# Optimization experiments

Measured on AMD Instinct MI355X. Metric: run time of the kernel, lower is better.

## Reference

```python
import jax, jax.numpy as jnp
import numpy as np


def setup_inputs() -> dict:
    key = jax.random.key(0)
    kq, kk, kv, km, kb = jax.random.split(key, 5)
    B, H, S, D = 4, 16, 2048, 64
    Q = jax.random.normal(kq, (B, H, S, D), dtype=jnp.float32)
    K = jax.random.normal(kk, (B, H, S, D), dtype=jnp.float32)
    V = jax.random.normal(kv, (B, H, S, D), dtype=jnp.float32)
    # key-padding style mask, broadcasts over query dim; 0 -> masked
    mask = jax.random.randint(km, (B, 1, 1, S), 0, 2, dtype=jnp.int32)
    attn_bias = jax.random.normal(kb, (1, H, S, S), dtype=jnp.float32)
    return {"Q": Q, "K": K, "V": V, "mask": mask, "attn_bias": attn_bias}


def reference(Q, K, V, mask, attn_bias):
    d_k = Q.shape[-1]
    scale = 1.0 / jnp.sqrt(jnp.asarray(d_k, Q.dtype))
    # [B,H,Sq,Sk] scores
    scores = jnp.einsum("bhqd,bhkd->bhqk", Q, K) * scale
    scores = scores + attn_bias
    scores = jnp.where(mask == 0, jnp.asarray(-1e9, scores.dtype), scores)
    attn = jax.nn.softmax(scores, axis=-1)
    # dropout is identity in eval/reference mode
    output = jnp.einsum("bhqk,bhkd->bhqd", attn, V)
    return output, attn
```

## Files before the change

### kernel.cpp

```cpp
#include <hip/hip_runtime.h>

#define NB 4
#define NH 16
#define NS 2048
#define ND 64
#define PST 2052

typedef __attribute__((ext_vector_type(8))) short short8;
typedef __attribute__((ext_vector_type(4))) short short4v;
typedef __attribute__((ext_vector_type(4))) float floatx4;
typedef __attribute__((ext_vector_type(2))) float floatx2;

__device__ __forceinline__ unsigned short f2bf(float f) {
  unsigned u = __builtin_bit_cast(unsigned, f);
  u = (u + 0x7FFFu + ((u >> 16) & 1u)) >> 16;
  return (unsigned short)u;
}
__device__ __forceinline__ float bf2f(unsigned short s) {
  unsigned u = ((unsigned)s) << 16;
  return __builtin_bit_cast(float, u);
}

__global__ __launch_bounds__(256) void prep_k_kernel(const float* __restrict__ K,
                                                     unsigned short* __restrict__ kb) {
  size_t i = ((size_t)blockIdx.x * 256 + threadIdx.x) * 4;
  floatx4 v = *(const floatx4*)(K + i);
  unsigned long long o = 0;
  o |= (unsigned long long)f2bf(v[0]);
  o |= (unsigned long long)f2bf(v[1]) << 16;
  o |= (unsigned long long)f2bf(v[2]) << 32;
  o |= (unsigned long long)f2bf(v[3]) << 48;
  *(unsigned long long*)(kb + i) = o;
}

__global__ __launch_bounds__(256) void prep_vt_kernel(const float* __restrict__ V,
                                                      unsigned short* __restrict__ vt) {
  __shared__ float tile[64][65];
  int kc = blockIdx.x & 31;
  int bh = blockIdx.x >> 5;
  int k0 = kc * 64;
  const float* src = V + ((size_t)bh * NS + k0) * ND;
  int t = threadIdx.x;
  int r0 = t >> 4;
  int c = (t & 15) * 4;
  for (int rr = 0; rr < 4; ++rr) {
    int r = rr * 16 + r0;
    floatx4 v = *(const floatx4*)(src + (size_t)r * ND + c);
    tile[r][c + 0] = v[0]; tile[r][c + 1] = v[1];
    tile[r][c + 2] = v[2]; tile[r][c + 3] = v[3];
  }
  __syncthreads();
  unsigned short* dst = vt + (size_t)bh * ND * NS + k0;
  for (int i = 0; i < 16; ++i) {
    int lin = i * 256 + t;
    int d = lin >> 6, k = lin & 63;
    dst[(size_t)d * NS + k] = f2bf(tile[k][d]);
  }
}

__global__ __launch_bounds__(1024, 8) void attn_kernel(
    const float* __restrict__ Q,
    const unsigned short* __restrict__ Kb,
    const unsigned short* __restrict__ VT,
    const int* __restrict__ mask,
    const float* __restrict__ bias,
    float* __restrict__ out,
    float* __restrict__ attn) {
  extern __shared__ char smem[];
  unsigned short* P = (unsigned short*)smem;
  float* sums = (float*)(smem + 16 * PST * 2);

  const int bid = blockIdx.x;
  const int b = bid & 3;
  const int qt = (bid >> 2) & 127;
  const int h = bid >> 9;
  const int q0 = qt * 16;

  const int tid = threadIdx.x;
  const int wave = tid >> 6;
  const int lane = tid & 63;
  const int lg = lane >> 4;
  const int lc = lane & 15;
  const int lg4 = lg * 4;
  const int lg8 = lg * 8;

  const size_t bh = (size_t)(b * NH + h);

  short8 aq[2];
  {
    const float* qrow = Q + (bh * NS + (size_t)(q0 + lc)) * ND + lg8;
#pragma unroll
    for (int t = 0; t < 2; ++t) {
      floatx4 f0 = *(const floatx4*)(qrow + t * 32);
      floatx4 f1 = *(const floatx4*)(qrow + t * 32 + 4);
      short8 a;
      a[0] = (short)f2bf(f0[0]); a[1] = (short)f2bf(f0[1]);
      a[2] = (short)f2bf(f0[2]); a[3] = (short)f2bf(f0[3]);
      a[4] = (short)f2bf(f1[0]); a[5] = (short)f2bf(f1[1]);
      a[6] = (short)f2bf(f1[2]); a[7] = (short)f2bf(f1[3]);
      aq[t] = a;
    }
  }

  const unsigned short* kp = Kb + bh * NS * ND + (size_t)lc * ND + lg8;
  const float* bprow = bias + ((size_t)h * NS + (size_t)(q0 + lg4)) * NS + lc;
  const int* mp = mask + b * NS + lc;

  float psum[4] = {0.f, 0.f, 0.f, 0.f};
  const int kb0 = wave * 128;

  short8 kfa[2], kfb[2];
  float bvv[2][4];
  int mvv[2];
  {
    const int k0 = kb0;
    kfa[0] = *(const short8*)(kp + (size_t)k0 * ND);
    kfb[0] = *(const short8*)(kp + (size_t)k0 * ND + 32);
    mvv[0] = mp[k0];
#pragma unroll
    for (int r = 0; r < 4; ++r) bvv[0][r] = bprow[(size_t)r * NS + k0];
  }
#pragma unroll
  for (int it = 0; it < 8; ++it) {
    const int cur = it & 1, nxt = cur ^ 1;
    if (it < 7) {
      const int k1 = kb0 + (it + 1) * 16;
      kfa[nxt] = *(const short8*)(kp + (size_t)k1 * ND);
      kfb[nxt] = *(const short8*)(kp + (size_t)k1 * ND + 32);
      mvv[nxt] = mp[k1];
#pragma unroll
      for (int r = 0; r < 4; ++r) bvv[nxt][r] = bprow[(size_t)r * NS + k1];
    }
    const int k0 = kb0 + it * 16;
    floatx4 c = {0.f, 0.f, 0.f, 0.f};
    c = __builtin_amdgcn_mfma_f32_16x16x32_bf16(aq[0], kfa[cur], c, 0, 0, 0);
    c = __builtin_amdgcn_mfma_f32_16x16x32_bf16(aq[1], kfb[cur], c, 0, 0, 0);
#pragma unroll
    for (int r = 0; r < 4; ++r) {
      float s = c[r] * 0.125f + bvv[cur][r];
      float p = mvv[cur] ? __expf(s) : 0.f;
      psum[r] += p;
      P[(lg4 + r) * PST + k0 + lc] = f2bf(p);
    }
  }

#pragma unroll
  for (int r = 0; r < 4; ++r) {
    float v = psum[r];
    v += __shfl_xor(v, 1);
    v += __shfl_xor(v, 2);
    v += __shfl_xor(v, 4);
    v += __shfl_xor(v, 8);
    if (lc == 0) sums[wave * 16 + lg4 + r] = v;
  }
  __syncthreads();

  {
    const int row = wave;
    float tot = 0.f;
#pragma unroll
    for (int w = 0; w < 16; ++w) tot += sums[w * 16 + row];
    const float inv = 1.f / tot;
    float* arow = attn + (bh * NS + (size_t)(q0 + row)) * NS;
    const unsigned short* prow = P + row * PST;
#pragma unroll
    for (int it = 0; it < 8; ++it) {
      const int col = it * 256 + lane * 4;
      short4v pv = *(const short4v*)(prow + col);
      floatx4 f;
      f[0] = bf2f((unsigned short)pv[0]) * inv;
      f[1] = bf2f((unsigned short)pv[1]) * inv;
      f[2] = bf2f((unsigned short)pv[2]) * inv;
      f[3] = bf2f((unsigned short)pv[3]) * inv;
      __builtin_nontemporal_store(f, (floatx4*)(arow + col));
    }
  }

  floatx4 o[4];
#pragma unroll
  for (int dt = 0; dt < 4; ++dt) o[dt] = (floatx4){0.f, 0.f, 0.f, 0.f};

  const unsigned short* vp = VT + bh * (size_t)ND * NS + (size_t)lc * NS + lg8;
#pragma unroll
  for (int it = 0; it < 4; ++it) {
    const int k0 = kb0 + it * 32;
    const unsigned short* pr = P + lc * PST + k0 + lg8;
    short4v lo = *(const short4v*)pr;
    short4v hi = *(const short4v*)(pr + 4);
    short8 pa = __builtin_shufflevector(lo, hi, 0, 1, 2, 3, 4, 5, 6, 7);
#pragma unroll
    for (int dt = 0; dt < 4; ++dt) {
      short8 bb = *(const short8*)(vp + (size_t)(dt * 16) * NS + k0);
      o[dt] = __builtin_amdgcn_mfma_f32_16x16x32_bf16(pa, bb, o[dt], 0, 0, 0);
    }
  }
  __syncthreads();

  float* Ored = (float*)smem;
#pragma unroll
  for (int dt = 0; dt < 4; ++dt)
#pragma unroll
    for (int r = 0; r < 4; ++r)
      Ored[((size_t)wave * 16 + lg4 + r) * 64 + dt * 16 + lc] = o[dt][r];
  __syncthreads();

  {
    const int q = tid >> 6;
    const int col = tid & 63;
    float acc = 0.f;
#pragma unroll
    for (int w = 0; w < 16; ++w) acc += Ored[((size_t)w * 16 + q) * 64 + col];
    float tot = 0.f;
#pragma unroll
    for (int w = 0; w < 16; ++w) tot += sums[w * 16 + q];
    const float inv = 1.f / tot;
    __builtin_nontemporal_store(acc * inv, out + (bh * NS + (size_t)(q0 + q)) * ND + col);
  }
}

extern "C" void kernel_launch(void* const* d_in, const int* in_sizes, int n_in,
                              void* d_out, int out_size, void* d_ws, size_t ws_size,
                              hipStream_t stream) {
  const float* Q = (const float*)d_in[0];
  const float* K = (const float*)d_in[1];
  const float* V = (const float*)d_in[2];
  const int* mask = (const int*)d_in[3];
  const float* bias = (const float*)d_in[4];

  float* out = (float*)d_out;
  float* attn = out + (size_t)NB * NH * NS * ND;

  unsigned short* kb = (unsigned short*)d_ws;
  unsigned short* vt = kb + (size_t)NB * NH * NS * ND;

  const int lds_bytes = 16 * PST * 2 + 16 * 16 * 4;
  (void)hipFuncSetAttribute((const void*)attn_kernel,
                            hipFuncAttributeMaxDynamicSharedMemorySize, lds_bytes);

  prep_k_kernel<<<(NB * NH * NS * ND) / (256 * 4), 256, 0, stream>>>(K, kb);
  prep_vt_kernel<<<NB * NH * (NS / 64), 256, 0, stream>>>(V, vt);
  attn_kernel<<<NB * NH * (NS / 16), 1024, lds_bytes, stream>>>(Q, kb, vt, mask, bias, out, attn);
}
```

Baseline: 738.8 us.

## Halve waves per block, deepen K prefetch, interleave attn writes with PV MFMAs

The attention kernel now launches 512 threads (8 waves) per block, so each wave covers 256 keys instead of 128. The score loop uses a 4-slot register ring that prefetches K, bias and mask three steps ahead, where it used to double-buffer. The normalized attention-row stores are interleaved with the P·V MFMAs and double-buffered V^T loads, so the attn write stream overlaps compute. The final reduction reads 8 partials and writes two floats per thread. The trade-off is higher register pressure per wave and fewer waves per block to hide latency.

```diff
diff --git a/kernel.cpp b/kernel.cpp
--- a/kernel.cpp
+++ b/kernel.cpp
@@ -58,7 +58,7 @@
   }
 }
 
-__global__ __launch_bounds__(1024, 8) void attn_kernel(
+__global__ __launch_bounds__(512, 4) void attn_kernel(
     const float* __restrict__ Q,
     const unsigned short* __restrict__ Kb,
     const unsigned short* __restrict__ VT,
@@ -105,40 +105,47 @@
   const unsigned short* kp = Kb + bh * NS * ND + (size_t)lc * ND + lg8;
   const float* bprow = bias + ((size_t)h * NS + (size_t)(q0 + lg4)) * NS + lc;
   const int* mp = mask + b * NS + lc;
+  const int kb0 = wave * 256;
 
   float psum[4] = {0.f, 0.f, 0.f, 0.f};
-  const int kb0 = wave * 128;
-
-  short8 kfa[2], kfb[2];
-  float bvv[2][4];
-  int mvv[2];
-  {
-    const int k0 = kb0;
-    kfa[0] = *(const short8*)(kp + (size_t)k0 * ND);
-    kfb[0] = *(const short8*)(kp + (size_t)k0 * ND + 32);
-    mvv[0] = mp[k0];
-#pragma unroll
-    for (int r = 0; r < 4; ++r) bvv[0][r] = bprow[(size_t)r * NS + k0];
-  }
-#pragma unroll
-  for (int it = 0; it < 8; ++it) {
-    const int cur = it & 1, nxt = cur ^ 1;
-    if (it < 7) {
-      const int k1 = kb0 + (it + 1) * 16;
-      kfa[nxt] = *(const short8*)(kp + (size_t)k1 * ND);
-      kfb[nxt] = *(const short8*)(kp + (size_t)k1 * ND + 32);
-      mvv[nxt] = mp[k1];
-#pragma unroll
-      for (int r = 0; r < 4; ++r) bvv[nxt][r] = bprow[(size_t)r * NS + k1];
+
+  short8 rka[4], rkb[4];
+  floatx4 rbv[4];
+  int rmv[4];
+#pragma unroll
+  for (int i = 0; i < 3; ++i) {
+    const int k0 = kb0 + i * 16;
+    rka[i] = *(const short8*)(kp + (size_t)k0 * ND);
+    rkb[i] = *(const short8*)(kp + (size_t)k0 * ND + 32);
+    rmv[i] = mp[k0];
+    floatx4 bv;
+#pragma unroll
+    for (int r = 0; r < 4; ++r) bv[r] = bprow[(size_t)r * NS + k0];
+    rbv[i] = bv;
+  }
+#pragma unroll
+  for (int it = 0; it < 16; ++it) {
+    const int s = it & 3;
+    if (it < 13) {
+      const int ps = (it + 3) & 3;
+      const int k1 = kb0 + (it + 3) * 16;
+      rka[ps] = *(const short8*)(kp + (size_t)k1 * ND);
+      rkb[ps] = *(const short8*)(kp + (size_t)k1 * ND + 32);
+      rmv[ps] = mp[k1];
+      floatx4 bv;
+#pragma unroll
+      for (int r = 0; r < 4; ++r) bv[r] = bprow[(size_t)r * NS + k1];
+      rbv[ps] = bv;
     }
     const int k0 = kb0 + it * 16;
     floatx4 c = {0.f, 0.f, 0.f, 0.f};
-    c = __builtin_amdgcn_mfma_f32_16x16x32_bf16(aq[0], kfa[cur], c, 0, 0, 0);
-    c = __builtin_amdgcn_mfma_f32_16x16x32_bf16(aq[1], kfb[cur], c, 0, 0, 0);
+    c = __builtin_amdgcn_mfma_f32_16x16x32_bf16(aq[0], rka[s], c, 0, 0, 0);
+    c = __builtin_amdgcn_mfma_f32_16x16x32_bf16(aq[1], rkb[s], c, 0, 0, 0);
+    const int mv = rmv[s];
 #pragma unroll
     for (int r = 0; r < 4; ++r) {
-      float s = c[r] * 0.125f + bvv[cur][r];
-      float p = mvv[cur] ? __expf(s) : 0.f;
+      float sc = c[r] * 0.125f + rbv[s][r];
+      float p = mv ? __expf(sc) : 0.f;
       psum[r] += p;
       P[(lg4 + r) * PST + k0 + lc] = f2bf(p);
     }
@@ -155,25 +162,34 @@
   }
   __syncthreads();
 
+  const int wrow0 = wave * 2;
+  float inv0, inv1;
   {
-    const int row = wave;
-    float tot = 0.f;
-#pragma unroll
-    for (int w = 0; w < 16; ++w) tot += sums[w * 16 + row];
-    const float inv = 1.f / tot;
-    float* arow = attn + (bh * NS + (size_t)(q0 + row)) * NS;
-    const unsigned short* prow = P + row * PST;
-#pragma unroll
-    for (int it = 0; it < 8; ++it) {
-      const int col = it * 256 + lane * 4;
-      short4v pv = *(const short4v*)(prow + col);
-      floatx4 f;
-      f[0] = bf2f((unsigned short)pv[0]) * inv;
-      f[1] = bf2f((unsigned short)pv[1]) * inv;
-      f[2] = bf2f((unsigned short)pv[2]) * inv;
-      f[3] = bf2f((unsigned short)pv[3]) * inv;
-      __builtin_nontemporal_store(f, (floatx4*)(arow + col));
-    }
+    float t0 = 0.f, t1 = 0.f;
+#pragma unroll
+    for (int w = 0; w < 8; ++w) {
+      t0 += sums[w * 16 + wrow0];
+      t1 += sums[w * 16 + wrow0 + 1];
+    }
+    inv0 = 1.f / t0;
+    inv1 = 1.f / t1;
+  }
+
+  const size_t abase = (bh * NS + (size_t)q0) * NS;
+
+#define WRITECHUNK(c)                                                        \
+  {                                                                          \
+    const int row_ = wrow0 + ((c) >> 3);                                     \
+    const float inv_ = (((c) >> 3) == 0) ? inv0 : inv1;                      \
+    const int col_ = ((c) & 7) * 256 + lane * 4;                             \
+    short4v pv_ = *(const short4v*)(P + row_ * PST + col_);                  \
+    floatx4 f_;                                                              \
+    f_[0] = bf2f((unsigned short)pv_[0]) * inv_;                             \
+    f_[1] = bf2f((unsigned short)pv_[1]) * inv_;                             \
+    f_[2] = bf2f((unsigned short)pv_[2]) * inv_;                             \
+    f_[3] = bf2f((unsigned short)pv_[3]) * inv_;                             \
+    __builtin_nontemporal_store(f_, (floatx4*)(attn + abase +                \
+                                               (size_t)row_ * NS + col_));   \
   }
 
   floatx4 o[4];
@@ -181,19 +197,49 @@
   for (int dt = 0; dt < 4; ++dt) o[dt] = (floatx4){0.f, 0.f, 0.f, 0.f};
 
   const unsigned short* vp = VT + bh * (size_t)ND * NS + (size_t)lc * NS + lg8;
-#pragma unroll
-  for (int it = 0; it < 4; ++it) {
-    const int k0 = kb0 + it * 32;
-    const unsigned short* pr = P + lc * PST + k0 + lg8;
-    short4v lo = *(const short4v*)pr;
-    short4v hi = *(const short4v*)(pr + 4);
-    short8 pa = __builtin_shufflevector(lo, hi, 0, 1, 2, 3, 4, 5, 6, 7);
-#pragma unroll
-    for (int dt = 0; dt < 4; ++dt) {
-      short8 bb = *(const short8*)(vp + (size_t)(dt * 16) * NS + k0);
-      o[dt] = __builtin_amdgcn_mfma_f32_16x16x32_bf16(pa, bb, o[dt], 0, 0, 0);
-    }
-  }
+  short8 vt0[4], vt1[4];
+#pragma unroll
+  for (int dt = 0; dt < 4; ++dt)
+    vt0[dt] = *(const short8*)(vp + (size_t)(dt * 16) * NS + kb0);
+
+#pragma unroll
+  for (int ih = 0; ih < 4; ++ih) {
+    const int itA = ih * 2, itB = ih * 2 + 1;
+    const int k0A = kb0 + itA * 32, k0B = kb0 + itB * 32;
+#pragma unroll
+    for (int dt = 0; dt < 4; ++dt)
+      vt1[dt] = *(const short8*)(vp + (size_t)(dt * 16) * NS + k0B);
+    WRITECHUNK(ih * 4 + 0);
+    WRITECHUNK(ih * 4 + 1);
+    {
+      const unsigned short* pr = P + lc * PST + k0A + lg8;
+      short4v lo = *(const short4v*)pr;
+      short4v hi = *(const short4v*)(pr + 4);
+      short8 pa = __builtin_shufflevector(lo, hi, 0, 1, 2, 3, 4, 5, 6, 7);
+#pragma unroll
+      for (int dt = 0; dt < 4; ++dt)
+        o[dt] = __builtin_amdgcn_mfma_f32_16x16x32_bf16(pa, vt0[dt], o[dt], 0, 0, 0);
+    }
+    if (ih < 3) {
+      const int k0N = kb0 + (ih + 1) * 64;
+#pragma unroll
+      for (int dt = 0; dt < 4; ++dt)
+        vt0[dt] = *(const short8*)(vp + (size_t)(dt * 16) * NS + k0N);
+    }
+    WRITECHUNK(ih * 4 + 2);
+    WRITECHUNK(ih * 4 + 3);
+    {
+      const unsigned short* pr = P + lc * PST + k0B + lg8;
+      short4v lo = *(const short4v*)pr;
+      short4v hi = *(const short4v*)(pr + 4);
+      short8 pa = __builtin_shufflevector(lo, hi, 0, 1, 2, 3, 4, 5, 6, 7);
+#pragma unroll
+      for (int dt = 0; dt < 4; ++dt)
+        o[dt] = __builtin_amdgcn_mfma_f32_16x16x32_bf16(pa, vt1[dt], o[dt], 0, 0, 0);
+    }
+  }
+#undef WRITECHUNK
+
   __syncthreads();
 
   float* Ored = (float*)smem;
@@ -205,16 +251,23 @@
   __syncthreads();
 
   {
-    const int q = tid >> 6;
-    const int col = tid & 63;
-    float acc = 0.f;
-#pragma unroll
-    for (int w = 0; w < 16; ++w) acc += Ored[((size_t)w * 16 + q) * 64 + col];
+    const int q = tid >> 5;
+    const int c2 = (tid & 31) * 2;
+    floatx2 acc = {0.f, 0.f};
+#pragma unroll
+    for (int w = 0; w < 8; ++w) {
+      const float* p = Ored + ((size_t)w * 16 + q) * 64 + c2;
+      acc[0] += p[0];
+      acc[1] += p[1];
+    }
     float tot = 0.f;
 #pragma unroll
-    for (int w = 0; w < 16; ++w) tot += sums[w * 16 + q];
+    for (int w = 0; w < 8; ++w) tot += sums[w * 16 + q];
     const float inv = 1.f / tot;
-    __builtin_nontemporal_store(acc * inv, out + (bh * NS + (size_t)(q0 + q)) * ND + col);
+    floatx2 res;
+    res[0] = acc[0] * inv;
+    res[1] = acc[1] * inv;
+    __builtin_nontemporal_store(res, (floatx2*)(out + (bh * NS + (size_t)(q0 + q)) * ND + c2));
   }
 }
 
@@ -233,11 +286,11 @@
   unsigned short* kb = (unsigned short*)d_ws;
   unsigned short* vt = kb + (size_t)NB * NH * NS * ND;
 
-  const int lds_bytes = 16 * PST * 2 + 16 * 16 * 4;
+  const int lds_bytes = 16 * PST * 2 + 8 * 16 * 4;
   (void)hipFuncSetAttribute((const void*)attn_kernel,
                             hipFuncAttributeMaxDynamicSharedMemorySize, lds_bytes);
 
   prep_k_kernel<<<(NB * NH * NS * ND) / (256 * 4), 256, 0, stream>>>(K, kb);
   prep_vt_kernel<<<NB * NH * (NS / 64), 256, 0, stream>>>(V, vt);
-  attn_kernel<<<NB * NH * (NS / 16), 1024, lds_bytes, stream>>>(Q, kb, vt, mask, bias, out, attn);
-}
+  attn_kernel<<<NB * NH * (NS / 16), 512, lds_bytes, stream>>>(Q, kb, vt, mask, bias, out, attn);
+}
```

After: 634.4 us. 1.16x faster.
